# Kernel optimization log

Hardware: AMD Instinct MI355X
Metric: run time of the kernel (lower is better)

## Reference

```python
import jax, jax.numpy as jnp
import numpy as np

N_NODES = 50000
N_EDGES = 800000
N_GRAPHS = 1000
IN_CH = 78
HID = 128
EPS = 1e-5


def _mean_aggr(x, src, dst, n):
    # scatter-mean of source-node features onto destination nodes
    s = jax.ops.segment_sum(x[src], dst, num_segments=n)
    deg = jax.ops.segment_sum(jnp.ones((src.shape[0],), x.dtype), dst, num_segments=n)
    return s / jnp.maximum(deg, 1.0)[:, None]


def _sage(x, src, dst, W_n, b_n, W_r):
    # PyG SAGEConv (mean): lin_l(mean_j x_j) + lin_r(x_i); lin_l has bias
    agg = _mean_aggr(x, src, dst, x.shape[0])
    return agg @ W_n + b_n + x @ W_r


def _bn(x, gamma, beta):
    # training-mode BatchNorm1d over node dimension (biased variance)
    mu = jnp.mean(x, axis=0)
    var = jnp.mean((x - mu) ** 2, axis=0)
    return (x - mu) * jax.lax.rsqrt(var + EPS) * gamma + beta


def setup_inputs() -> dict:
    key = jax.random.key(0)
    ks = jax.random.split(key, 20)
    d = {}
    d["x"] = jax.random.normal(ks[0], (N_NODES, IN_CH), dtype=jnp.float32)
    d["edge_index"] = jax.random.randint(ks[1], (2, N_EDGES), 0, N_NODES, dtype=jnp.int64)
    d["batch"] = jnp.sort(jax.random.randint(ks[2], (N_NODES,), 0, N_GRAPHS, dtype=jnp.int64))
    dims = [(IN_CH, HID), (HID, HID), (HID, HID)]
    for i, (di, do) in enumerate(dims):
        d[f"W_n{i}"] = jax.random.normal(ks[3 + 4 * i], (di, do), dtype=jnp.float32) * 0.05
        d[f"b{i}"] = jnp.zeros((do,), dtype=jnp.float32)
        d[f"W_r{i}"] = jax.random.normal(ks[4 + 4 * i], (di, do), dtype=jnp.float32) * 0.05
        d[f"g{i}"] = jnp.ones((do,), dtype=jnp.float32)
        d[f"be{i}"] = jnp.zeros((do,), dtype=jnp.float32)
    d["Wh1"] = jax.random.normal(ks[16], (HID, HID // 2), dtype=jnp.float32) * 0.05
    d["bh1"] = jnp.zeros((HID // 2,), dtype=jnp.float32)
    d["Wh2"] = jax.random.normal(ks[17], (HID // 2, 1), dtype=jnp.float32) * 0.05
    d["bh2"] = jnp.zeros((1,), dtype=jnp.float32)
    return d


def reference(x, edge_index, batch,
              W_n0, b0, W_r0, g0, be0,
              W_n1, b1, W_r1, g1, be1,
              W_n2, b2, W_r2, g2, be2,
              Wh1, bh1, Wh2, bh2):
    src, dst = edge_index[0], edge_index[1]
    layers = [(W_n0, b0, W_r0, g0, be0), (W_n1, b1, W_r1, g1, be1), (W_n2, b2, W_r2, g2, be2)]
    h = x
    for W_n, b_n, W_r, gamma, beta in layers:
        h = jax.nn.relu(_bn(_sage(h, src, dst, W_n, b_n, W_r), gamma, beta))
    # global mean pool per graph: [N_GRAPHS, HID]
    s = jax.ops.segment_sum(h, batch, num_segments=N_GRAPHS)
    cnt = jax.ops.segment_sum(jnp.ones((h.shape[0],), h.dtype), batch, num_segments=N_GRAPHS)
    pooled = s / jnp.maximum(cnt, 1.0)[:, None]
    return jax.nn.relu(pooled @ Wh1 + bh1) @ Wh2 + bh2
```

## Files before the change

kernel.cpp:

```cpp
#include <hip/hip_runtime.h>
#include <hip/hip_bf16.h>
#include <math.h>

#define HID 128
#define NSB 128
#define NBLK_BIN 256
#define BINC_CAP 6144

typedef short short8 __attribute__((ext_vector_type(8)));
typedef float f32x4 __attribute__((ext_vector_type(4)));

__global__ void prep_kernel(const float* __restrict__ x, float* __restrict__ xp,
                            int* __restrict__ bcnt, int nbuck16,
                            const float* __restrict__ Wn0, const float* __restrict__ Wr0,
                            const float* __restrict__ Wn1, const float* __restrict__ Wr1,
                            const float* __restrict__ Wn2, const float* __restrict__ Wr2,
                            unsigned short* __restrict__ B0h, unsigned short* __restrict__ B0l,
                            unsigned short* __restrict__ B1h, unsigned short* __restrict__ B1l,
                            unsigned short* __restrict__ B2h, unsigned short* __restrict__ B2l,
                            int N, int K0, int K0pad) {
    int i = blockIdx.x * blockDim.x + threadIdx.x;
    if (i < nbuck16) bcnt[i] = 0;
    if (i < N * K0pad) {
        int row = i / K0pad;
        int c = i - row * K0pad;
        xp[i] = (c < K0) ? x[(size_t)row * K0 + c] : 0.f;
    }
    int n0 = 256 * K0pad, n1 = 256 * HID;
    if (i < n0 + 2 * n1) {
        const float *Wn, *Wr;
        unsigned short *bh, *bl;
        int K, idx;
        if (i < n0) { Wn = Wn0; Wr = Wr0; bh = B0h; bl = B0l; K = K0; idx = i; }
        else if (i < n0 + n1) { Wn = Wn1; Wr = Wr1; bh = B1h; bl = B1l; K = HID; idx = i - n0; }
        else { Wn = Wn2; Wr = Wr2; bh = B2h; bl = B2l; K = HID; idx = i - n0 - n1; }
        int j = idx & 7;
        int lane = (idx >> 3) & 63;
        int cb = (idx >> 9) & 15;
        int ks = idx >> 13;
        int k = ks * 32 + ((lane >> 4) & 3) * 8 + j;
        int ch = 16 * cb + (lane & 15);
        float v = 0.f;
        if (k < K) v = (ch < 128) ? Wn[k * 128 + ch] : Wr[k * 128 + (ch - 128)];
        __hip_bfloat16 h = __float2bfloat16(v);
        float hf = __bfloat162float(h);
        __hip_bfloat16 l = __float2bfloat16(v - hf);
        bh[idx] = *(unsigned short*)&h;
        bl[idx] = *(unsigned short*)&l;
    }
}

__global__ void binA_kernel(const int* __restrict__ dst, int* __restrict__ bcnt,
                            int ne, int nbuck, int shift) {
    __shared__ int hist[512];
    int t = threadIdx.x;
    for (int i = t; i < 512; i += 256) hist[i] = 0;
    __syncthreads();
    size_t beg = (size_t)ne * blockIdx.x / NBLK_BIN;
    size_t end = (size_t)ne * (blockIdx.x + 1) / NBLK_BIN;
    for (size_t e = beg + t; e < end; e += 256)
        atomicAdd(&hist[dst[e] >> shift], 1);
    __syncthreads();
    for (int b = t; b < nbuck; b += 256) {
        int h = hist[b];
        if (h) atomicAdd(&bcnt[b * 16], h);
    }
}

__global__ __launch_bounds__(512) void bucket_scan_kernel(const int* __restrict__ bcnt,
                                                          int* __restrict__ bbase,
                                                          int* __restrict__ bcur, int nbuck) {
    __shared__ int tmp[512];
    int t = threadIdx.x;
    int v = (t < nbuck) ? bcnt[t * 16] : 0;
    tmp[t] = v;
    __syncthreads();
    for (int off = 1; off < 512; off <<= 1) {
        int u = 0;
        if (t >= off) u = tmp[t - off];
        __syncthreads();
        if (t >= off) tmp[t] += u;
        __syncthreads();
    }
    if (t < nbuck) {
        int exc = tmp[t] - v;
        bbase[t] = exc;
        bcur[t * 16] = exc;
        if (t == nbuck - 1) bbase[nbuck] = tmp[t];
    }
}

__global__ void binB_kernel(const int* __restrict__ src, const int* __restrict__ dst,
                            int* __restrict__ bcur, uint2* __restrict__ ebuf,
                            int ne, int nbuck, int shift) {
    __shared__ int hist[512];
    __shared__ int base[512];
    int t = threadIdx.x;
    for (int i = t; i < 512; i += 256) hist[i] = 0;
    __syncthreads();
    size_t beg = (size_t)ne * blockIdx.x / NBLK_BIN;
    size_t end = (size_t)ne * (blockIdx.x + 1) / NBLK_BIN;
    for (size_t e = beg + t; e < end; e += 256)
        atomicAdd(&hist[dst[e] >> shift], 1);
    __syncthreads();
    for (int b = t; b < nbuck; b += 256) {
        int h = hist[b];
        if (h) base[b] = atomicAdd(&bcur[b * 16], h);
        hist[b] = 0;
    }
    __syncthreads();
    for (size_t e = beg + t; e < end; e += 256) {
        int d = dst[e];
        int bk = d >> shift;
        int r = atomicAdd(&hist[bk], 1);
        ebuf[base[bk] + r] = make_uint2((unsigned)src[e], (unsigned)d);
    }
}

__global__ __launch_bounds__(512) void binC_kernel(const uint2* __restrict__ ebuf,
                                                   const int* __restrict__ bbase,
                                                   int* __restrict__ counts,
                                                   int* __restrict__ offsets,
                                                   int* __restrict__ esrc,
                                                   int N, int shift) {
    __shared__ int cnt[512], tmp[512], cur[512];
    __shared__ int sout[BINC_CAP];
    int b = blockIdx.x;
    int t = threadIdx.x;
    int node0 = b << shift;
    int npb = 1 << shift;
    if (node0 + npb > N) npb = N - node0;
    int ebase = bbase[b];
    int eend = bbase[b + 1];
    int total = eend - ebase;
    cnt[t] = 0;
    __syncthreads();
    for (int e = ebase + t; e < eend; e += 512)
        atomicAdd(&cnt[ebuf[e].y - node0], 1);
    __syncthreads();
    int v = cnt[t];
    tmp[t] = v;
    __syncthreads();
    for (int off = 1; off < 512; off <<= 1) {
        int u = 0;
        if (t >= off) u = tmp[t - off];
        __syncthreads();
        if (t >= off) tmp[t] += u;
        __syncthreads();
    }
    int exc = tmp[t] - v;
    cur[t] = exc;
    if (t < npb) {
        counts[node0 + t] = v;
        offsets[node0 + t] = ebase + exc;
    }
    __syncthreads();
    if (total <= BINC_CAP) {
        for (int e = ebase + t; e < eend; e += 512) {
            uint2 p = ebuf[e];
            int r = atomicAdd(&cur[(int)p.y - node0], 1);
            sout[r] = (int)p.x;
        }
        __syncthreads();
        for (int k = t; k < total; k += 512)
            esrc[ebase + k] = sout[k];
    } else {
        for (int e = ebase + t; e < eend; e += 512) {
            uint2 p = ebuf[e];
            int r = atomicAdd(&cur[(int)p.y - node0], 1);
            esrc[ebase + r] = (int)p.x;
        }
    }
}

template <int KPAD>
__global__ __launch_bounds__(256) void gemm_kernel(
    const float* __restrict__ A,
    const float* __restrict__ psum, const float* __restrict__ psumsq,
    const float* __restrict__ g, const float* __restrict__ be,
    const unsigned short* __restrict__ Bswh, const unsigned short* __restrict__ Bswl,
    unsigned short* __restrict__ U16, float* __restrict__ V, int N) {
    constexpr int LSTR = KPAD + 8;
    constexpr int KSTEPS = KPAD / 32;
    constexpr int ITERS = (32 * KPAD) / 1024;
    int tid = threadIdx.x;
    int lane = tid & 63;
    int w = tid >> 6;
    int q = lane >> 4;
    int m = lane & 15;
    int n0 = blockIdx.x * 32;
    int apply_bn = (psum != nullptr);

    __shared__ float s_sc[HID], s_sh[HID];
    __shared__ unsigned short sA_h[32 * LSTR], sA_l[32 * LSTR];
    if (apply_bn) {
        if (tid < HID) {
            double S = 0.0, Q = 0.0;
            for (int b = 0; b < NSB; b++) {
                S += (double)psum[b * HID + tid];
                Q += (double)psumsq[b * HID + tid];
            }
            double mu = S / (double)N;
            double var = Q / (double)N - mu * mu;
            if (var < 0.0) var = 0.0;
            float rs = (float)(1.0 / sqrt(var + 1e-5));
            float sc = g[tid] * rs;
            s_sc[tid] = sc;
            s_sh[tid] = be[tid] - (float)mu * sc;
        }
        __syncthreads();
    }

    float4 zreg[ITERS];
#pragma unroll
    for (int it = 0; it < ITERS; it++) {
        int idx = tid * 4 + it * 1024;
        int row = idx / KPAD;
        int col = idx - row * KPAD;
        int grow = n0 + row;
        if (grow >= N) grow = N - 1;
        zreg[it] = *(const float4*)(A + (size_t)grow * KPAD + col);
    }
#pragma unroll
    for (int it = 0; it < ITERS; it++) {
        int idx = tid * 4 + it * 1024;
        int row = idx / KPAD;
        int col = idx - row * KPAD;
        float y[4] = {zreg[it].x, zreg[it].y, zreg[it].z, zreg[it].w};
        if (apply_bn) {
#pragma unroll
            for (int j = 0; j < 4; j++)
                y[j] = fmaxf(fmaf(y[j], s_sc[col + j], s_sh[col + j]), 0.f);
        }
        ushort4 h4, l4;
        unsigned short* ph = (unsigned short*)&h4;
        unsigned short* pl = (unsigned short*)&l4;
#pragma unroll
        for (int j = 0; j < 4; j++) {
            __hip_bfloat16 h = __float2bfloat16(y[j]);
            float hf = __bfloat162float(h);
            __hip_bfloat16 lo = __float2bfloat16(y[j] - hf);
            ph[j] = *(unsigned short*)&h;
            pl[j] = *(unsigned short*)&lo;
        }
        *(ushort4*)&sA_h[row * LSTR + col] = h4;
        *(ushort4*)&sA_l[row * LSTR + col] = l4;
    }
    __syncthreads();

    f32x4 acc[2][4];
#pragma unroll
    for (int r = 0; r < 2; r++)
#pragma unroll
        for (int c = 0; c < 4; c++) acc[r][c] = (f32x4){0.f, 0.f, 0.f, 0.f};

#pragma unroll
    for (int ks = 0; ks < KSTEPS; ks++) {
        int ko = ks * 32 + q * 8;
        short8 ah[2], al[2], bh[4], bl[4];
#pragma unroll
        for (int c = 0; c < 4; c++) {
            int cb = 4 * w + c;
            size_t off = ((size_t)(ks * 16 + cb) * 64 + lane) * 8;
            bh[c] = __builtin_bit_cast(short8, *(const uint4*)(Bswh + off));
            bl[c] = __builtin_bit_cast(short8, *(const uint4*)(Bswl + off));
        }
#pragma unroll
        for (int r = 0; r < 2; r++) {
            int ao = (16 * r + m) * LSTR + ko;
            ah[r] = __builtin_bit_cast(short8, *(uint4*)&sA_h[ao]);
            al[r] = __builtin_bit_cast(short8, *(uint4*)&sA_l[ao]);
        }
#pragma unroll
        for (int r = 0; r < 2; r++)
#pragma unroll
            for (int c = 0; c < 4; c++) {
                acc[r][c] = __builtin_amdgcn_mfma_f32_16x16x32_bf16(ah[r], bh[c], acc[r][c], 0, 0, 0);
                acc[r][c] = __builtin_amdgcn_mfma_f32_16x16x32_bf16(ah[r], bl[c], acc[r][c], 0, 0, 0);
                acc[r][c] = __builtin_amdgcn_mfma_f32_16x16x32_bf16(al[r], bh[c], acc[r][c], 0, 0, 0);
            }
    }
    int colbase = (w & 1) * 64;
    if (w < 2) {
#pragma unroll
        for (int r = 0; r < 2; r++)
#pragma unroll
            for (int c = 0; c < 4; c++) {
                int col = colbase + 16 * c + m;
#pragma unroll
                for (int i = 0; i < 4; i++) {
                    int row = n0 + 16 * r + 4 * q + i;
                    if (row < N) {
                        __hip_bfloat16 h = __float2bfloat16(acc[r][c][i]);
                        U16[(size_t)row * HID + col] = *(unsigned short*)&h;
                    }
                }
            }
    } else {
#pragma unroll
        for (int r = 0; r < 2; r++)
#pragma unroll
            for (int c = 0; c < 4; c++) {
                int col = colbase + 16 * c + m;
#pragma unroll
                for (int i = 0; i < 4; i++) {
                    int row = n0 + 16 * r + 4 * q + i;
                    if (row < N) V[(size_t)row * HID + col] = acc[r][c][i];
                }
            }
    }
}

__global__ __launch_bounds__(256) void agg_kernel(const unsigned short* __restrict__ U16,
                                                  const float* __restrict__ V,
                                                  const float* __restrict__ bias,
                                                  const int* __restrict__ counts,
                                                  const int* __restrict__ offsets,
                                                  const int* __restrict__ esrc,
                                                  float* __restrict__ Z, int N) {
    int grp = threadIdx.x >> 5;
    int l32 = threadIdx.x & 31;
    int n = blockIdx.x * 8 + grp;
    if (n >= N) return;
    int deg = counts[n];
    int st = offsets[n];
    int co = 4 * l32;

    auto cvt = [](uint2 raw) -> f32x4 {
        f32x4 v;
        v[0] = __uint_as_float(raw.x << 16);
        v[1] = __uint_as_float(raw.x & 0xffff0000u);
        v[2] = __uint_as_float(raw.y << 16);
        v[3] = __uint_as_float(raw.y & 0xffff0000u);
        return v;
    };

    f32x4 a0 = {0,0,0,0}, a1 = {0,0,0,0}, a2 = {0,0,0,0}, a3 = {0,0,0,0};
    f32x4 a4 = {0,0,0,0}, a5 = {0,0,0,0}, a6 = {0,0,0,0}, a7 = {0,0,0,0};
    int i = 0;
    for (; i + 7 < deg; i += 8) {
        int s0 = esrc[st + i + 0], s1 = esrc[st + i + 1];
        int s2 = esrc[st + i + 2], s3 = esrc[st + i + 3];
        int s4 = esrc[st + i + 4], s5 = esrc[st + i + 5];
        int s6 = esrc[st + i + 6], s7 = esrc[st + i + 7];
        uint2 r0 = *(const uint2*)(U16 + (size_t)s0 * HID + co);
        uint2 r1 = *(const uint2*)(U16 + (size_t)s1 * HID + co);
        uint2 r2 = *(const uint2*)(U16 + (size_t)s2 * HID + co);
        uint2 r3 = *(const uint2*)(U16 + (size_t)s3 * HID + co);
        uint2 r4 = *(const uint2*)(U16 + (size_t)s4 * HID + co);
        uint2 r5 = *(const uint2*)(U16 + (size_t)s5 * HID + co);
        uint2 r6 = *(const uint2*)(U16 + (size_t)s6 * HID + co);
        uint2 r7 = *(const uint2*)(U16 + (size_t)s7 * HID + co);
        a0 += cvt(r0); a1 += cvt(r1); a2 += cvt(r2); a3 += cvt(r3);
        a4 += cvt(r4); a5 += cvt(r5); a6 += cvt(r6); a7 += cvt(r7);
    }
    for (; i + 3 < deg; i += 4) {
        int s0 = esrc[st + i + 0], s1 = esrc[st + i + 1];
        int s2 = esrc[st + i + 2], s3 = esrc[st + i + 3];
        uint2 r0 = *(const uint2*)(U16 + (size_t)s0 * HID + co);
        uint2 r1 = *(const uint2*)(U16 + (size_t)s1 * HID + co);
        uint2 r2 = *(const uint2*)(U16 + (size_t)s2 * HID + co);
        uint2 r3 = *(const uint2*)(U16 + (size_t)s3 * HID + co);
        a0 += cvt(r0); a1 += cvt(r1); a2 += cvt(r2); a3 += cvt(r3);
    }
    for (; i < deg; i++) {
        uint2 r0 = *(const uint2*)(U16 + (size_t)esrc[st + i] * HID + co);
        a0 += cvt(r0);
    }
    f32x4 acc = ((a0 + a1) + (a2 + a3)) + ((a4 + a5) + (a6 + a7));
    float d = (float)(deg > 1 ? deg : 1);
    f32x4 vv = ((const f32x4*)V)[(size_t)n * 32 + l32];
    f32x4 bb = ((const f32x4*)bias)[l32];
    ((f32x4*)Z)[(size_t)n * 32 + l32] = acc / d + vv + bb;
}

__global__ __launch_bounds__(256) void stats_kernel(const float* __restrict__ Z,
                                                    float* __restrict__ psum,
                                                    float* __restrict__ psumsq, int N) {
    int t = threadIdx.x;
    int cq = t & 31;
    int rg = t >> 5;
    const f32x4* Z4 = (const f32x4*)Z;
    f32x4 s = {0,0,0,0}, q = {0,0,0,0};
    for (int n = blockIdx.x * 8 + rg; n < N; n += NSB * 8) {
        f32x4 z = Z4[(size_t)n * 32 + cq];
        s += z;
        q += z * z;
    }
    __shared__ f32x4 bs[256], bq[256];
    bs[t] = s;
    bq[t] = q;
    __syncthreads();
#pragma unroll
    for (int off = 4; off > 0; off >>= 1) {
        if (rg < off) {
            bs[t] += bs[t + off * 32];
            bq[t] += bq[t + off * 32];
        }
        __syncthreads();
    }
    if (rg == 0) {
        ((f32x4*)psum)[blockIdx.x * 32 + cq] = bs[t];
        ((f32x4*)psumsq)[blockIdx.x * 32 + cq] = bq[t];
    }
}

__global__ __launch_bounds__(128) void pool_head_kernel(const float* __restrict__ Z,
                                                        const float* __restrict__ psum,
                                                        const float* __restrict__ psumsq,
                                                        const float* __restrict__ g,
                                                        const float* __restrict__ be,
                                                        const int* __restrict__ batch,
                                                        const float* __restrict__ Wh1,
                                                        const float* __restrict__ bh1,
                                                        const float* __restrict__ Wh2,
                                                        const float* __restrict__ bh2,
                                                        float* __restrict__ out, int N) {
    int gph = blockIdx.x;
    __shared__ int bounds[2];
    __shared__ float p[128];
    int t = threadIdx.x;
    if (t < 2) {
        int target = gph + t;
        int lo = 0, hi = N;
        while (lo < hi) {
            int mid = (lo + hi) >> 1;
            if (batch[mid] < target) lo = mid + 1;
            else hi = mid;
        }
        bounds[t] = lo;
    }
    double S = 0.0, Q = 0.0;
    for (int b = 0; b < NSB; b++) {
        S += (double)psum[b * HID + t];
        Q += (double)psumsq[b * HID + t];
    }
    double mu = S / (double)N;
    double var = Q / (double)N - mu * mu;
    if (var < 0.0) var = 0.0;
    float rs = (float)(1.0 / sqrt(var + 1e-5));
    float sc = g[t] * rs;
    float sh = be[t] - (float)mu * sc;
    __syncthreads();
    int start = bounds[0], end = bounds[1];
    float s = 0.f;
    for (int n = start; n < end; n++)
        s += fmaxf(fmaf(Z[(size_t)n * HID + t], sc, sh), 0.f);
    p[t] = s / fmaxf((float)(end - start), 1.f);
    __syncthreads();
    if (t < 64) {
        float acc = bh1[t];
        for (int k = 0; k < 128; k++) acc = fmaf(p[k], Wh1[k * 64 + t], acc);
        acc = fmaxf(acc, 0.f);
        float prod = acc * Wh2[t];
        for (int off = 32; off > 0; off >>= 1) prod += __shfl_down(prod, off);
        if (t == 0) out[gph] = prod + bh2[0];
    }
}

extern "C" void kernel_launch(void* const* d_in, const int* in_sizes, int n_in,
                              void* d_out, int out_size, void* d_ws, size_t ws_size,
                              hipStream_t stream) {
    const float* x = (const float*)d_in[0];
    const int* ei = (const int*)d_in[1];
    const int* batch = (const int*)d_in[2];
    const float* Wn[3] = {(const float*)d_in[3], (const float*)d_in[8], (const float*)d_in[13]};
    const float* bb[3] = {(const float*)d_in[4], (const float*)d_in[9], (const float*)d_in[14]};
    const float* Wr[3] = {(const float*)d_in[5], (const float*)d_in[10], (const float*)d_in[15]};
    const float* gg[3] = {(const float*)d_in[6], (const float*)d_in[11], (const float*)d_in[16]};
    const float* be[3] = {(const float*)d_in[7], (const float*)d_in[12], (const float*)d_in[17]};
    const float* Wh1 = (const float*)d_in[18];
    const float* bh1 = (const float*)d_in[19];
    const float* Wh2 = (const float*)d_in[20];
    const float* bh2 = (const float*)d_in[21];
    float* out = (float*)d_out;

    const int N = in_sizes[2];
    const int NE = in_sizes[1] / 2;
    const int NG = out_size;
    const int K0 = in_sizes[0] / N;
    const int K0pad = (K0 <= 96) ? 96 : 128;

    const int* src = ei;
    const int* dst = ei + NE;

    int shift = 7;
    int nbuck = (N + 127) >> 7;
    while (nbuck > 512) { shift++; nbuck = (N + (1 << shift) - 1) >> shift; }

    char* w = (char*)d_ws;
    auto alloc = [&](size_t bytes) -> void* {
        void* p = (void*)w;
        w += (bytes + 255) & ~(size_t)255;
        return p;
    };
    unsigned short* bufU16 = (unsigned short*)alloc((size_t)N * HID * 2);
    float* bufV = (float*)alloc((size_t)N * HID * 4);
    float* bufZ = (float*)alloc((size_t)N * HID * 4);
    float* xp = (float*)alloc((size_t)N * K0pad * 4);
    unsigned short* BTh[3];
    unsigned short* BTl[3];
    BTh[0] = (unsigned short*)alloc((size_t)256 * K0pad * 2);
    BTl[0] = (unsigned short*)alloc((size_t)256 * K0pad * 2);
    BTh[1] = (unsigned short*)alloc((size_t)256 * HID * 2);
    BTl[1] = (unsigned short*)alloc((size_t)256 * HID * 2);
    BTh[2] = (unsigned short*)alloc((size_t)256 * HID * 2);
    BTl[2] = (unsigned short*)alloc((size_t)256 * HID * 2);
    int* counts = (int*)alloc((size_t)N * 4);
    int* offsets = (int*)alloc((size_t)(N + 1) * 4);
    int* esrc = (int*)alloc((size_t)NE * 4);
    int* bcnt = (int*)alloc((size_t)512 * 16 * 4);
    int* bcur = (int*)alloc((size_t)512 * 16 * 4);
    int* bbase = (int*)alloc((size_t)(512 + 1) * 4);
    float* pstats = (float*)alloc((size_t)3 * 2 * NSB * HID * 4);
    uint2* ebuf = (uint2*)bufZ;
    (void)ws_size;
    (void)n_in;

    size_t prep_total = (size_t)N * K0pad;
    prep_kernel<<<(prep_total + 255) / 256, 256, 0, stream>>>(
        x, xp, bcnt, nbuck * 16, Wn[0], Wr[0], Wn[1], Wr[1], Wn[2], Wr[2],
        BTh[0], BTl[0], BTh[1], BTl[1], BTh[2], BTl[2], N, K0, K0pad);

    binA_kernel<<<NBLK_BIN, 256, 0, stream>>>(dst, bcnt, NE, nbuck, shift);
    bucket_scan_kernel<<<1, 512, 0, stream>>>(bcnt, bbase, bcur, nbuck);
    binB_kernel<<<NBLK_BIN, 256, 0, stream>>>(src, dst, bcur, ebuf, NE, nbuck, shift);
    binC_kernel<<<nbuck, 512, 0, stream>>>(ebuf, bbase, counts, offsets, esrc, N, shift);

    int gblocks = (N + 31) / 32;
    int ablocks = (N + 7) / 8;
    for (int l = 0; l < 3; l++) {
        const float* Ain = (l == 0) ? xp : bufZ;
        int Kpad = (l == 0) ? K0pad : HID;
        const float* ppsum = (l == 0) ? (const float*)nullptr : pstats + (size_t)(l - 1) * 2 * NSB * HID;
        const float* ppsq = (l == 0) ? (const float*)nullptr : pstats + (size_t)(l - 1) * 2 * NSB * HID + NSB * HID;
        const float* pg = (l == 0) ? (const float*)nullptr : gg[l - 1];
        const float* pb = (l == 0) ? (const float*)nullptr : be[l - 1];
        if (Kpad == 96)
            gemm_kernel<96><<<gblocks, 256, 0, stream>>>(Ain, ppsum, ppsq, pg, pb,
                                                         BTh[l], BTl[l], bufU16, bufV, N);
        else
            gemm_kernel<128><<<gblocks, 256, 0, stream>>>(Ain, ppsum, ppsq, pg, pb,
                                                          BTh[l], BTl[l], bufU16, bufV, N);
        agg_kernel<<<ablocks, 256, 0, stream>>>(bufU16, bufV, bb[l], counts, offsets, esrc, bufZ, N);
        stats_kernel<<<NSB, 256, 0, stream>>>(bufZ,
                                              pstats + (size_t)l * 2 * NSB * HID,
                                              pstats + (size_t)l * 2 * NSB * HID + NSB * HID, N);
    }

    pool_head_kernel<<<NG, 128, 0, stream>>>(bufZ,
                                             pstats + (size_t)2 * 2 * NSB * HID,
                                             pstats + (size_t)2 * 2 * NSB * HID + NSB * HID,
                                             gg[2], be[2], batch, Wh1, bh1, Wh2, bh2, out, N);
}
```

Baseline: 401.8 us.

## Finalize BN stats once per layer and load GEMM A-tiles directly from global

Adds a single-block kernel that reduces the per-block BatchNorm partial sums into scale/shift once per layer, instead of every GEMM block and every pooling block redoing the 128-way double-precision reduction. The GEMM no longer stages the A tile through shared memory with a barrier. Each lane instead loads its own 8 floats per k-step from global, applies BN+ReLU, and splits them into bf16 hi/lo fragments in registers. This removes LDS traffic, shared-memory footprint and a sync, but the four waves now each re-read the same A rows from global/L2 and redo the split conversion, and three extra tiny kernel launches are added.

Result: slower. 427.1 us (+6.3%).

```diff
diff --git a/kernel.cpp b/kernel.cpp
--- a/kernel.cpp
+++ b/kernel.cpp
@@ -173,80 +173,46 @@
     }
 }
 
+__global__ __launch_bounds__(128) void bnfin_kernel(const float* __restrict__ psum,
+                                                    const float* __restrict__ psumsq,
+                                                    const float* __restrict__ g,
+                                                    const float* __restrict__ be,
+                                                    float* __restrict__ scsh, int N) {
+    int t = threadIdx.x;
+    double S = 0.0, Q = 0.0;
+    for (int b = 0; b < NSB; b++) {
+        S += (double)psum[b * HID + t];
+        Q += (double)psumsq[b * HID + t];
+    }
+    double mu = S / (double)N;
+    double var = Q / (double)N - mu * mu;
+    if (var < 0.0) var = 0.0;
+    float rs = (float)(1.0 / sqrt(var + 1e-5));
+    float sc = g[t] * rs;
+    scsh[t] = sc;
+    scsh[HID + t] = be[t] - (float)mu * sc;
+}
+
 template <int KPAD>
 __global__ __launch_bounds__(256) void gemm_kernel(
     const float* __restrict__ A,
-    const float* __restrict__ psum, const float* __restrict__ psumsq,
-    const float* __restrict__ g, const float* __restrict__ be,
+    const float* __restrict__ scsh,
     const unsigned short* __restrict__ Bswh, const unsigned short* __restrict__ Bswl,
     unsigned short* __restrict__ U16, float* __restrict__ V, int N) {
-    constexpr int LSTR = KPAD + 8;
     constexpr int KSTEPS = KPAD / 32;
-    constexpr int ITERS = (32 * KPAD) / 1024;
     int tid = threadIdx.x;
     int lane = tid & 63;
     int w = tid >> 6;
     int q = lane >> 4;
     int m = lane & 15;
     int n0 = blockIdx.x * 32;
-    int apply_bn = (psum != nullptr);
-
-    __shared__ float s_sc[HID], s_sh[HID];
-    __shared__ unsigned short sA_h[32 * LSTR], sA_l[32 * LSTR];
-    if (apply_bn) {
-        if (tid < HID) {
-            double S = 0.0, Q = 0.0;
-            for (int b = 0; b < NSB; b++) {
-                S += (double)psum[b * HID + tid];
-                Q += (double)psumsq[b * HID + tid];
-            }
-            double mu = S / (double)N;
-            double var = Q / (double)N - mu * mu;
-            if (var < 0.0) var = 0.0;
-            float rs = (float)(1.0 / sqrt(var + 1e-5));
-            float sc = g[tid] * rs;
-            s_sc[tid] = sc;
-            s_sh[tid] = be[tid] - (float)mu * sc;
-        }
-        __syncthreads();
-    }
-
-    float4 zreg[ITERS];
-#pragma unroll
-    for (int it = 0; it < ITERS; it++) {
-        int idx = tid * 4 + it * 1024;
-        int row = idx / KPAD;
-        int col = idx - row * KPAD;
-        int grow = n0 + row;
-        if (grow >= N) grow = N - 1;
-        zreg[it] = *(const float4*)(A + (size_t)grow * KPAD + col);
-    }
-#pragma unroll
-    for (int it = 0; it < ITERS; it++) {
-        int idx = tid * 4 + it * 1024;
-        int row = idx / KPAD;
-        int col = idx - row * KPAD;
-        float y[4] = {zreg[it].x, zreg[it].y, zreg[it].z, zreg[it].w};
-        if (apply_bn) {
-#pragma unroll
-            for (int j = 0; j < 4; j++)
-                y[j] = fmaxf(fmaf(y[j], s_sc[col + j], s_sh[col + j]), 0.f);
-        }
-        ushort4 h4, l4;
-        unsigned short* ph = (unsigned short*)&h4;
-        unsigned short* pl = (unsigned short*)&l4;
-#pragma unroll
-        for (int j = 0; j < 4; j++) {
-            __hip_bfloat16 h = __float2bfloat16(y[j]);
-            float hf = __bfloat162float(h);
-            __hip_bfloat16 lo = __float2bfloat16(y[j] - hf);
-            ph[j] = *(unsigned short*)&h;
-            pl[j] = *(unsigned short*)&lo;
-        }
-        *(ushort4*)&sA_h[row * LSTR + col] = h4;
-        *(ushort4*)&sA_l[row * LSTR + col] = l4;
-    }
-    __syncthreads();
+    bool apply_bn = (scsh != nullptr);
+
+    int grow[2];
+    grow[0] = n0 + m;
+    grow[1] = n0 + 16 + m;
+    if (grow[0] >= N) grow[0] = N - 1;
+    if (grow[1] >= N) grow[1] = N - 1;
 
     f32x4 acc[2][4];
 #pragma unroll
@@ -257,7 +223,7 @@
 #pragma unroll
     for (int ks = 0; ks < KSTEPS; ks++) {
         int ko = ks * 32 + q * 8;
-        short8 ah[2], al[2], bh[4], bl[4];
+        short8 bh[4], bl[4];
 #pragma unroll
         for (int c = 0; c < 4; c++) {
             int cb = 4 * w + c;
@@ -265,11 +231,34 @@
             bh[c] = __builtin_bit_cast(short8, *(const uint4*)(Bswh + off));
             bl[c] = __builtin_bit_cast(short8, *(const uint4*)(Bswl + off));
         }
+        float scv[8], shv[8];
+        if (apply_bn) {
+            float4 s0 = *(const float4*)(scsh + ko);
+            float4 s1 = *(const float4*)(scsh + ko + 4);
+            float4 h0 = *(const float4*)(scsh + HID + ko);
+            float4 h1 = *(const float4*)(scsh + HID + ko + 4);
+            scv[0] = s0.x; scv[1] = s0.y; scv[2] = s0.z; scv[3] = s0.w;
+            scv[4] = s1.x; scv[5] = s1.y; scv[6] = s1.z; scv[7] = s1.w;
+            shv[0] = h0.x; shv[1] = h0.y; shv[2] = h0.z; shv[3] = h0.w;
+            shv[4] = h1.x; shv[5] = h1.y; shv[6] = h1.z; shv[7] = h1.w;
+        }
+        short8 ah[2], al[2];
 #pragma unroll
         for (int r = 0; r < 2; r++) {
-            int ao = (16 * r + m) * LSTR + ko;
-            ah[r] = __builtin_bit_cast(short8, *(uint4*)&sA_h[ao]);
-            al[r] = __builtin_bit_cast(short8, *(uint4*)&sA_l[ao]);
+            const float* ap = A + (size_t)grow[r] * KPAD + ko;
+            float4 z0 = *(const float4*)(ap);
+            float4 z1 = *(const float4*)(ap + 4);
+            float y[8] = {z0.x, z0.y, z0.z, z0.w, z1.x, z1.y, z1.z, z1.w};
+#pragma unroll
+            for (int j = 0; j < 8; j++) {
+                float yy = y[j];
+                if (apply_bn) yy = fmaxf(fmaf(yy, scv[j], shv[j]), 0.f);
+                __hip_bfloat16 h = __float2bfloat16(yy);
+                float hf = __bfloat162float(h);
+                __hip_bfloat16 lo = __float2bfloat16(yy - hf);
+                ah[r][j] = *(short*)&h;
+                al[r][j] = *(short*)&lo;
+            }
         }
 #pragma unroll
         for (int r = 0; r < 2; r++)
@@ -406,10 +395,7 @@
 }
 
 __global__ __launch_bounds__(128) void pool_head_kernel(const float* __restrict__ Z,
-                                                        const float* __restrict__ psum,
-                                                        const float* __restrict__ psumsq,
-                                                        const float* __restrict__ g,
-                                                        const float* __restrict__ be,
+                                                        const float* __restrict__ scsh,
                                                         const int* __restrict__ batch,
                                                         const float* __restrict__ Wh1,
                                                         const float* __restrict__ bh1,
@@ -430,17 +416,8 @@
         }
         bounds[t] = lo;
     }
-    double S = 0.0, Q = 0.0;
-    for (int b = 0; b < NSB; b++) {
-        S += (double)psum[b * HID + t];
-        Q += (double)psumsq[b * HID + t];
-    }
-    double mu = S / (double)N;
-    double var = Q / (double)N - mu * mu;
-    if (var < 0.0) var = 0.0;
-    float rs = (float)(1.0 / sqrt(var + 1e-5));
-    float sc = g[t] * rs;
-    float sh = be[t] - (float)mu * sc;
+    float sc = scsh[t];
+    float sh = scsh[HID + t];
     __syncthreads();
     int start = bounds[0], end = bounds[1];
     float s = 0.f;
@@ -513,6 +490,7 @@
     int* bcur = (int*)alloc((size_t)512 * 16 * 4);
     int* bbase = (int*)alloc((size_t)(512 + 1) * 4);
     float* pstats = (float*)alloc((size_t)3 * 2 * NSB * HID * 4);
+    float* scsh = (float*)alloc((size_t)3 * 2 * HID * 4);
     uint2* ebuf = (uint2*)bufZ;
     (void)ws_size;
     (void)n_in;
@@ -532,24 +510,22 @@
     for (int l = 0; l < 3; l++) {
         const float* Ain = (l == 0) ? xp : bufZ;
         int Kpad = (l == 0) ? K0pad : HID;
-        const float* ppsum = (l == 0) ? (const float*)nullptr : pstats + (size_t)(l - 1) * 2 * NSB * HID;
-        const float* ppsq = (l == 0) ? (const float*)nullptr : pstats + (size_t)(l - 1) * 2 * NSB * HID + NSB * HID;
-        const float* pg = (l == 0) ? (const float*)nullptr : gg[l - 1];
-        const float* pb = (l == 0) ? (const float*)nullptr : be[l - 1];
+        const float* pscsh = (l == 0) ? (const float*)nullptr : scsh + (size_t)(l - 1) * 2 * HID;
         if (Kpad == 96)
-            gemm_kernel<96><<<gblocks, 256, 0, stream>>>(Ain, ppsum, ppsq, pg, pb,
+            gemm_kernel<96><<<gblocks, 256, 0, stream>>>(Ain, pscsh,
                                                          BTh[l], BTl[l], bufU16, bufV, N);
         else
-            gemm_kernel<128><<<gblocks, 256, 0, stream>>>(Ain, ppsum, ppsq, pg, pb,
+            gemm_kernel<128><<<gblocks, 256, 0, stream>>>(Ain, pscsh,
                                                           BTh[l], BTl[l], bufU16, bufV, N);
         agg_kernel<<<ablocks, 256, 0, stream>>>(bufU16, bufV, bb[l], counts, offsets, esrc, bufZ, N);
         stats_kernel<<<NSB, 256, 0, stream>>>(bufZ,
                                               pstats + (size_t)l * 2 * NSB * HID,
                                               pstats + (size_t)l * 2 * NSB * HID + NSB * HID, N);
-    }
-
-    pool_head_kernel<<<NG, 128, 0, stream>>>(bufZ,
-                                             pstats + (size_t)2 * 2 * NSB * HID,
-                                             pstats + (size_t)2 * 2 * NSB * HID + NSB * HID,
-                                             gg[2], be[2], batch, Wh1, bh1, Wh2, bh2, out, N);
-}
+        bnfin_kernel<<<1, 128, 0, stream>>>(pstats + (size_t)l * 2 * NSB * HID,
+                                            pstats + (size_t)l * 2 * NSB * HID + NSB * HID,
+                                            gg[l], be[l], scsh + (size_t)l * 2 * HID, N);
+    }
+
+    pool_head_kernel<<<NG, 128, 0, stream>>>(bufZ, scsh + (size_t)2 * 2 * HID,
+                                             batch, Wh1, bh1, Wh2, bh2, out, N);
+}
```
